# Kernel tuning notes

Hardware: AMD Instinct MI355X
Metric: run time of the kernel (lower is better)

The kernel has to match this reference:

```python
import jax, jax.numpy as jnp
import numpy as np

N = 131072      # nodes
E = 2097152     # edges (avg degree 16)
G = 64          # graphs in batch
D_IN = 64       # input node feature dim
D_E = 2         # raw edge feature dim
H = 128         # hidden dim
OUT = 128       # output dim
L = 3           # num GCN layers
GDIM = 6        # global feature dim
GP = H // 4     # global proj dim = 32
EPS = 1e-5      # BatchNorm eps


def setup_inputs() -> dict:
    key = jax.random.key(0)
    ks = jax.random.split(key, 24)
    s = lambda d: 1.0 / np.sqrt(d)
    return {
        "x": jax.random.normal(ks[0], (N, D_IN), jnp.float32),
        "edge_attr_raw": jax.random.normal(ks[1], (E, D_E), jnp.float32),
        "global_x": jax.random.normal(ks[2], (G, GDIM), jnp.float32),
        "W_in": jax.random.normal(ks[3], (D_IN, H), jnp.float32) * s(D_IN),
        "b_in": jnp.zeros((H,), jnp.float32),
        "W_edge": jax.random.normal(ks[4], (D_E, H), jnp.float32) * s(D_E),
        "b_edge": jnp.zeros((H,), jnp.float32),
        "W_gcn": jax.random.normal(ks[5], (L, H, H), jnp.float32) * s(H),
        "b_gcn": jnp.zeros((L, H), jnp.float32),
        "bn_gamma": jnp.ones((L, H), jnp.float32),
        "bn_beta": jnp.zeros((L, H), jnp.float32),
        "bn_mean": jax.random.normal(ks[6], (L, H), jnp.float32) * 0.1,
        "bn_var": jnp.ones((L, H), jnp.float32) + 0.1 * jax.random.uniform(ks[7], (L, H), jnp.float32),
        "W_gproj": jax.random.normal(ks[8], (GDIM, GP), jnp.float32) * s(GDIM),
        "b_gproj": jnp.zeros((GP,), jnp.float32),
        "W_gcomb": jax.random.normal(ks[9], (H + GP, OUT), jnp.float32) * s(H + GP),
        "b_gcomb": jnp.zeros((OUT,), jnp.float32),
        "row": jax.random.randint(ks[10], (E,), 0, N, jnp.int32),
        "col": jax.random.randint(ks[11], (E,), 0, N, jnp.int32),
        "batch": jnp.sort(jax.random.randint(ks[12], (N,), 0, G, jnp.int32)),
    }


def reference(x, edge_attr_raw, global_x, W_in, b_in, W_edge, b_edge,
              W_gcn, b_gcn, bn_gamma, bn_beta, bn_mean, bn_var,
              W_gproj, b_gproj, W_gcomb, b_gcomb, row, col, batch):
    n = x.shape[0]
    h = x @ W_in + b_in                                   # [N,H]
    ea = edge_attr_raw @ W_edge + b_edge                  # [E,H]
    ones_e = jnp.ones((row.shape[0],), h.dtype)
    deg = jnp.clip(jax.ops.segment_sum(ones_e, row, num_segments=n), 1.0)[:, None]
    for i in range(L):
        msg = h[col] * ea                                 # gather + edge weight [E,H]
        agg = jax.ops.segment_sum(msg, row, num_segments=n) / deg  # scatter-add + norm
        h = h + agg
        h = h @ W_gcn[i] + b_gcn[i]
        # eval-mode BatchNorm (running stats); dropout is identity in eval
        h = (h - bn_mean[i]) * (bn_gamma[i] / jnp.sqrt(bn_var[i] + EPS)) + bn_beta[i]
        h = jax.nn.relu(h)
    # global mean pool per graph
    gsum = jax.ops.segment_sum(h, batch, num_segments=G)
    gcnt = jnp.clip(jax.ops.segment_sum(jnp.ones((n,), h.dtype), batch, num_segments=G), 1.0)[:, None]
    g = gsum / gcnt                                       # [G,H]
    gp = jax.nn.relu(global_x @ W_gproj + b_gproj)        # [G,H//4]
    return jnp.concatenate([g, gp], axis=1) @ W_gcomb + b_gcomb  # [G,OUT]
```

## Files before the change

kernel.cpp:

```cpp
#include <hip/hip_runtime.h>
#include <stdint.h>

#define N_NODES 131072
#define N_EDGES 2097152
#define NG 64
#define HD 128
#define NL 3
#define EPSB 1e-5f

#define BUCKETS 256
#define BSHIFT 9
#define ROWS_PB 512
#define CHUNK 8192
#define NCHUNK (N_EDGES / CHUNK)
#define PAD_SLACK (7 * ROWS_PB)
#define CSR_CAP (N_EDGES + BUCKETS * (PAD_SLACK + 8))
#define TPAD 68

typedef unsigned short ushort_t;
typedef __bf16 bf16x8 __attribute__((ext_vector_type(8)));
typedef float f32x4 __attribute__((ext_vector_type(4)));

__device__ __forceinline__ float bf2f(uint32_t u16) {
    union { uint32_t i; float f; } c; c.i = u16 << 16; return c.f;
}
__device__ __forceinline__ float lo2f(uint32_t u) {
    union { uint32_t i; float f; } c; c.i = u << 16; return c.f;
}
__device__ __forceinline__ float hi2f(uint32_t u) {
    union { uint32_t i; float f; } c; c.i = u & 0xffff0000u; return c.f;
}
__device__ __forceinline__ ushort_t f2bf(float f) {
    union { float f; uint32_t i; } c; c.f = f;
    uint32_t u = c.i;
    uint32_t r = (u + 0x7fffu + ((u >> 16) & 1u)) >> 16;
    return (ushort_t)r;
}
__device__ __forceinline__ float ldf(const void* p, int i, int isb) {
    return isb ? bf2f(((const ushort_t*)p)[i]) : ((const float*)p)[i];
}

__global__ void detect_k(const uint32_t* __restrict__ ea, int* __restrict__ flag) {
    __shared__ int sm[256];
    int t = threadIdx.x;
    int plaus = 0;
    for (int j = 0; j < 16; j++) {
        uint32_t w = ea[t * 16 + j];
        uint32_t e0 = (w >> 7) & 0xFF;
        uint32_t e1 = (w >> 23) & 0xFF;
        plaus += (e0 >= 100 && e0 <= 140) ? 1 : 0;
        plaus += (e1 >= 100 && e1 <= 140) ? 1 : 0;
    }
    sm[t] = plaus;
    __syncthreads();
    for (int o = 128; o > 0; o >>= 1) {
        if (t < o) sm[t] += sm[t + o];
        __syncthreads();
    }
    if (t == 0) flag[0] = (sm[0] * 10 >= 8192 * 9) ? 1 : 0;
}

__global__ void prep_bn(const void* gamma, const void* beta,
                        const void* mean, const void* var,
                        const void* bgcn, float* sc, float* sh,
                        const int* __restrict__ flag) {
    int isb = flag[0];
    int i = blockIdx.x * 128 + threadIdx.x;
    if (i < NL * HD) {
        float g = ldf(gamma, i, isb), b = ldf(beta, i, isb);
        float m = ldf(mean, i, isb), v = ldf(var, i, isb), bb = ldf(bgcn, i, isb);
        float s = g / sqrtf(v + EPSB);
        sc[i] = s;
        sh[i] = (bb - m) * s + b;
    }
}

__global__ void transpose_k(const void* __restrict__ W, ushort_t* __restrict__ WTg,
                            const int* __restrict__ flag) {
    int isb = flag[0];
    int idx = blockIdx.x * 256 + threadIdx.x;
    if (idx < NL * HD * HD) {
        int l = idx >> 14;
        int rem = idx & 16383;
        int k = rem >> 7, n = rem & 127;
        WTg[l * 16384 + n * 128 + k] = f2bf(ldf(W, idx, isb));
    }
}

__global__ __launch_bounds__(256) void bucketA_k(
    const int* __restrict__ row, const int* __restrict__ col,
    const void* __restrict__ ea_raw,
    uint2* __restrict__ staged, uint32_t* __restrict__ cntmat,
    uint32_t* __restrict__ offmat, const int* __restrict__ flag)
{
    __shared__ int hist[256], offs[256], offs_ex[256], cur[256];
    int isb = flag[0];
    int t = threadIdx.x;
    int base = blockIdx.x * CHUNK;
    hist[t] = 0;
    __syncthreads();
#pragma unroll 4
    for (int j = 0; j < 32; j++) {
        int r = row[base + j * 256 + t];
        atomicAdd(&hist[r >> BSHIFT], 1);
    }
    __syncthreads();
    int v = hist[t];
    offs[t] = v;
    __syncthreads();
    for (int o = 1; o < 256; o <<= 1) {
        int u = (t >= o) ? offs[t - o] : 0;
        __syncthreads();
        offs[t] += u;
        __syncthreads();
    }
    offs_ex[t] = offs[t] - v;
    cur[t] = 0;
    cntmat[blockIdx.x * 256 + t] = (uint32_t)v;
    offmat[blockIdx.x * 256 + t] = (uint32_t)(offs[t] - v);
    __syncthreads();
    uint2* slice = staged + (size_t)blockIdx.x * CHUNK;
    for (int j = 0; j < 32; j++) {
        int e = base + j * 256 + t;
        int r = row[e];
        int b = r >> BSHIFT;
        uint32_t packed;
        if (isb) {
            packed = ((const uint32_t*)ea_raw)[e];
        } else {
            const float* f = (const float*)ea_raw + (size_t)e * 2;
            packed = (uint32_t)f2bf(f[0]) | ((uint32_t)f2bf(f[1]) << 16);
        }
        int pos = offs_ex[b] + atomicAdd(&cur[b], 1);
        slice[pos] = make_uint2((uint32_t)(((r & (ROWS_PB - 1)) << 17) | col[e]), packed);
    }
}

__global__ __launch_bounds__(256) void bucketsum_k(const uint32_t* __restrict__ cntmat,
                                                   uint32_t* __restrict__ btot) {
    __shared__ int sm[256];
    int b = blockIdx.x, t = threadIdx.x;
    sm[t] = (int)cntmat[t * 256 + b];
    __syncthreads();
    for (int o = 128; o > 0; o >>= 1) {
        if (t < o) sm[t] += sm[t + o];
        __syncthreads();
    }
    if (t == 0) btot[b] = (uint32_t)sm[0];
}

__global__ __launch_bounds__(256) void scan2_k(const uint32_t* __restrict__ btot,
                                               uint32_t* __restrict__ bbase) {
    __shared__ int sm[256];
    int t = threadIdx.x;
    int v = ((int)btot[t] + PAD_SLACK + 7) & ~7;
    sm[t] = v;
    __syncthreads();
    for (int o = 1; o < 256; o <<= 1) {
        int u = (t >= o) ? sm[t - o] : 0;
        __syncthreads();
        sm[t] += u;
        __syncthreads();
    }
    bbase[t] = (uint32_t)(sm[t] - v);
}

__global__ __launch_bounds__(512) void buildB_k(
    const uint2* __restrict__ staged, const uint32_t* __restrict__ cntmat,
    const uint32_t* __restrict__ offmat, const uint32_t* __restrict__ bbase,
    uint2* __restrict__ csr, int* __restrict__ csr_off, int* __restrict__ deg)
{
    __shared__ int runoff[257];
    __shared__ int runstart[256];
    __shared__ int hist2[512];
    __shared__ int po[512];
    __shared__ int cur2[512];
    int b = blockIdx.x, t = threadIdx.x;

    int myc = 0;
    if (t < 256) {
        myc = (int)cntmat[t * 256 + b];
        runstart[t] = t * CHUNK + (int)offmat[t * 256 + b];
        runoff[t] = myc;
    }
    __syncthreads();
    for (int o = 1; o < 256; o <<= 1) {
        int u = 0;
        if (t < 256 && t >= o) u = runoff[t - o];
        __syncthreads();
        if (t < 256) runoff[t] += u;
        __syncthreads();
    }
    if (t < 256) {
        int incl = runoff[t];
        runoff[t] = incl - myc;
        if (t == 255) runoff[256] = incl;
    }
    hist2[t] = 0;
    cur2[t] = 0;
    __syncthreads();
    int T = runoff[256];

    for (int i = t; i < T; i += 512) {
        int lo = 0, hi = 255;
        while (lo < hi) { int mid = (lo + hi + 1) >> 1; if (runoff[mid] <= i) lo = mid; else hi = mid - 1; }
        uint32_t x = staged[runstart[lo] + (i - runoff[lo])].x;
        atomicAdd(&hist2[x >> 17], 1);
    }
    __syncthreads();

    int pv = (hist2[t] + 7) & ~7;
    po[t] = pv;
    __syncthreads();
    for (int o = 1; o < 512; o <<= 1) {
        int u = (t >= o) ? po[t - o] : 0;
        __syncthreads();
        po[t] += u;
        __syncthreads();
    }
    po[t] -= pv;
    __syncthreads();

    int gbase = (int)bbase[b];
    csr_off[b * ROWS_PB + t] = gbase + po[t];
    deg[b * ROWS_PB + t] = hist2[t];

    for (int i = t; i < T; i += 512) {
        int lo = 0, hi = 255;
        while (lo < hi) { int mid = (lo + hi + 1) >> 1; if (runoff[mid] <= i) lo = mid; else hi = mid - 1; }
        uint2 en = staged[runstart[lo] + (i - runoff[lo])];
        int r = en.x >> 17;
        int pos = po[r] + atomicAdd(&cur2[r], 1);
        csr[gbase + pos] = make_uint2(en.x & 0x1FFFFu, en.y);
    }
    __syncthreads();
    int d = hist2[t], p = (d + 7) & ~7;
    for (int k = d; k < p; k++) csr[gbase + po[t] + k] = make_uint2(N_NODES, 0u);
}

__global__ __launch_bounds__(64, 4) void layer_fused_k(
    const uint32_t* __restrict__ h32,
    const int* __restrict__ csr_off, const int* __restrict__ degv,
    const uint2* __restrict__ csr,
    const void* __restrict__ Wedge, const void* __restrict__ bedge,
    const ushort_t* __restrict__ WTg,
    const float* __restrict__ sc, const float* __restrict__ sh,
    ushort_t* __restrict__ Hout,
    const int* __restrict__ flag)
{
    __shared__ uint32_t tile[16 * TPAD];
    int isb = flag[0];
    int lane = threadIdx.x;
    int quad = lane >> 4, l16 = lane & 15;
    int nodebase = blockIdx.x * 16;

    float w0x = ldf(Wedge, 2 * lane, isb),       w0y = ldf(Wedge, 2 * lane + 1, isb);
    float w1x = ldf(Wedge, 128 + 2 * lane, isb), w1y = ldf(Wedge, 128 + 2 * lane + 1, isb);
    float bex = ldf(bedge, 2 * lane, isb),       bey = ldf(bedge, 2 * lane + 1, isb);

    int dg = degv[nodebase];
    int st = csr_off[nodebase];
    for (int i = 0; i < 16; i++) {
        int dgn = 0, stn = 0;
        if (i < 15) {
            dgn = degv[nodebase + i + 1];
            stn = csr_off[nodebase + i + 1];
        }
        uint32_t hn = h32[(uint32_t)(nodebase + i) * 64 + lane];

        int nit = (dg + 7) >> 3;
        const uint4* gp = (const uint4*)csr + (st >> 1);
        float ax = 0.f, ay = 0.f;
        int it = 0;
        for (; it + 2 <= nit; it += 2) {
            uint4 q0 = gp[0], q1 = gp[1], q2 = gp[2], q3 = gp[3];
            uint4 q4 = gp[4], q5 = gp[5], q6 = gp[6], q7 = gp[7];
            gp += 8;
            uint32_t cols[16] = {q0.x, q0.z, q1.x, q1.z, q2.x, q2.z, q3.x, q3.z,
                                 q4.x, q4.z, q5.x, q5.z, q6.x, q6.z, q7.x, q7.z};
            uint32_t eav[16]  = {q0.y, q0.w, q1.y, q1.w, q2.y, q2.w, q3.y, q3.w,
                                 q4.y, q4.w, q5.y, q5.w, q6.y, q6.w, q7.y, q7.w};
            uint32_t hv[16];
#pragma unroll
            for (int j = 0; j < 16; j++) hv[j] = h32[cols[j] * 64 + lane];
#pragma unroll
            for (int j = 0; j < 16; j++) {
                float a0 = bf2f(eav[j] & 0xffffu);
                float a1 = bf2f(eav[j] >> 16);
                float ex = fmaf(a1, w1x, fmaf(a0, w0x, bex));
                float ey = fmaf(a1, w1y, fmaf(a0, w0y, bey));
                ax = fmaf(lo2f(hv[j]), ex, ax);
                ay = fmaf(hi2f(hv[j]), ey, ay);
            }
        }
        if (it < nit) {
            uint4 q0 = gp[0], q1 = gp[1], q2 = gp[2], q3 = gp[3];
            uint32_t cols[8] = {q0.x, q0.z, q1.x, q1.z, q2.x, q2.z, q3.x, q3.z};
            uint32_t eav[8]  = {q0.y, q0.w, q1.y, q1.w, q2.y, q2.w, q3.y, q3.w};
            uint32_t hv[8];
#pragma unroll
            for (int j = 0; j < 8; j++) hv[j] = h32[cols[j] * 64 + lane];
#pragma unroll
            for (int j = 0; j < 8; j++) {
                float a0 = bf2f(eav[j] & 0xffffu);
                float a1 = bf2f(eav[j] >> 16);
                float ex = fmaf(a1, w1x, fmaf(a0, w0x, bex));
                float ey = fmaf(a1, w1y, fmaf(a0, w0y, bey));
                ax = fmaf(lo2f(hv[j]), ex, ax);
                ay = fmaf(hi2f(hv[j]), ey, ay);
            }
        }
        float inv = 1.0f / (float)(dg > 0 ? dg : 1);
        float tx = lo2f(hn) + ax * inv;
        float ty = hi2f(hn) + ay * inv;
        tile[i * TPAD + lane] = (uint32_t)f2bf(tx) | ((uint32_t)f2bf(ty) << 16);
        dg = dgn; st = stn;
    }

    f32x4 acc[8];
#pragma unroll
    for (int c = 0; c < 8; c++) acc[c] = (f32x4){0.f, 0.f, 0.f, 0.f};

#pragma unroll
    for (int kk = 0; kk < 4; kk++) {
        bf16x8 a = *(const bf16x8*)(tile + l16 * TPAD + kk * 16 + quad * 4);
#pragma unroll
        for (int c = 0; c < 8; c++) {
            bf16x8 b = *(const bf16x8*)(WTg + (c * 16 + l16) * 128 + kk * 32 + quad * 8);
            acc[c] = __builtin_amdgcn_mfma_f32_16x16x32_bf16(a, b, acc[c], 0, 0, 0);
        }
    }
#pragma unroll
    for (int c = 0; c < 8; c++) {
        int gcol = c * 16 + l16;
        float s = sc[gcol], o = sh[gcol];
#pragma unroll
        for (int r = 0; r < 4; r++) {
            float v = fmaxf(fmaf(acc[c][r], s, o), 0.f);
            Hout[(size_t)(nodebase + quad * 4 + r) * 128 + gcol] = f2bf(v);
        }
    }
}

__global__ __launch_bounds__(256) void gemm_in_k(
    const void* __restrict__ X, const void* __restrict__ W,
    const void* __restrict__ bin, ushort_t* __restrict__ Hout,
    const int* __restrict__ flag)
{
    __shared__ ushort_t WT[128 * 72];
    int isb = flag[0];
    int tid = threadIdx.x;
    for (int idx = tid; idx < 64 * 128; idx += 256) {
        int k = idx >> 7, n = idx & 127;
        WT[n * 72 + k] = f2bf(ldf(W, idx, isb));
    }
    __syncthreads();
    int wave = tid >> 6, lane = tid & 63;
    int quad = lane >> 4, l16 = lane & 15;
    int row = blockIdx.x * 64 + wave * 16 + l16;

    f32x4 acc[8];
#pragma unroll
    for (int c = 0; c < 8; c++) acc[c] = (f32x4){0.f, 0.f, 0.f, 0.f};

#pragma unroll
    for (int kk = 0; kk < 2; kk++) {
        int aoff = row * 64 + kk * 32 + quad * 8;
        union { bf16x8 v; ushort_t s[8]; } a;
        if (isb) {
            a.v = *(const bf16x8*)((const ushort_t*)X + aoff);
        } else {
            const float* xf = (const float*)X + aoff;
            f32x4 p0 = *(const f32x4*)xf;
            f32x4 p1 = *(const f32x4*)(xf + 4);
#pragma unroll
            for (int j = 0; j < 4; j++) { a.s[j] = f2bf(p0[j]); a.s[4 + j] = f2bf(p1[j]); }
        }
#pragma unroll
        for (int c = 0; c < 8; c++) {
            bf16x8 b = *(const bf16x8*)(&WT[(c * 16 + l16) * 72 + kk * 32 + quad * 8]);
            acc[c] = __builtin_amdgcn_mfma_f32_16x16x32_bf16(a.v, b, acc[c], 0, 0, 0);
        }
    }
    int rbase = blockIdx.x * 64 + wave * 16 + quad * 4;
#pragma unroll
    for (int c = 0; c < 8; c++) {
        int gcol = c * 16 + l16;
        float bb = ldf(bin, gcol, isb);
#pragma unroll
        for (int r = 0; r < 4; r++) {
            Hout[(rbase + r) * 128 + gcol] = f2bf(acc[c][r] + bb);
        }
    }
}

__global__ __launch_bounds__(128) void pool_k(
    const ushort_t* __restrict__ Hf, const int* __restrict__ batch,
    float* __restrict__ gsum, int* __restrict__ gcnt)
{
    int t = threadIdx.x;
    int n0 = blockIdx.x * 256;
    int n1 = n0 + 256;
    int cur = batch[n0];
    float s = 0.f; int c = 0;
    for (int n = n0; n < n1; n++) {
        int g = batch[n];
        if (g != cur) {
            atomicAdd(&gsum[cur * 128 + t], s);
            if (t == 0) atomicAdd(&gcnt[cur], c);
            s = 0.f; c = 0; cur = g;
        }
        s += bf2f(Hf[n * 128 + t]);
        c++;
    }
    atomicAdd(&gsum[cur * 128 + t], s);
    if (t == 0) atomicAdd(&gcnt[cur], c);
}

__global__ __launch_bounds__(128) void final_k(
    const float* __restrict__ gsum, const int* __restrict__ gcnt,
    const void* __restrict__ gx, const void* __restrict__ Wgp,
    const void* __restrict__ bgp, const void* __restrict__ Wgc,
    const void* __restrict__ bgc, void* __restrict__ out,
    const int* __restrict__ flag)
{
    __shared__ float gm[160];
    int isb = flag[0];
    int g = blockIdx.x, t = threadIdx.x;
    int c = gcnt[g]; if (c < 1) c = 1;
    gm[t] = gsum[g * 128 + t] / (float)c;
    if (t < 32) {
        float a = ldf(bgp, t, isb);
        for (int d = 0; d < 6; d++) a += ldf(gx, g * 6 + d, isb) * ldf(Wgp, d * 32 + t, isb);
        gm[128 + t] = fmaxf(a, 0.f);
    }
    __syncthreads();
    float a = ldf(bgc, t, isb);
    for (int k = 0; k < 160; k++) a += gm[k] * ldf(Wgc, k * 128 + t, isb);
    if (isb) ((ushort_t*)out)[g * 128 + t] = f2bf(a);
    else     ((float*)out)[g * 128 + t] = a;
}

extern "C" void kernel_launch(void* const* d_in, const int* in_sizes, int n_in,
                              void* d_out, int out_size, void* d_ws, size_t ws_size,
                              hipStream_t stream) {
    const void* x       = d_in[0];
    const void* ea_raw  = d_in[1];
    const void* gx      = d_in[2];
    const void* W_in    = d_in[3];
    const void* b_in    = d_in[4];
    const void* W_edge  = d_in[5];
    const void* b_edge  = d_in[6];
    const void* W_gcn   = d_in[7];
    const void* b_gcn   = d_in[8];
    const void* bn_g    = d_in[9];
    const void* bn_b    = d_in[10];
    const void* bn_m    = d_in[11];
    const void* bn_v    = d_in[12];
    const void* W_gproj = d_in[13];
    const void* b_gproj = d_in[14];
    const void* W_gcomb = d_in[15];
    const void* b_gcomb = d_in[16];
    const int* row   = (const int*)d_in[17];
    const int* col   = (const int*)d_in[18];
    const int* batch = (const int*)d_in[19];

    char* ws = (char*)d_ws;
    size_t off = 0;
    float*    gsum    = (float*)(ws + off);    off += (size_t)NG * HD * 4;
    int*      gcnt    = (int*)(ws + off);      off += 256;
    size_t zero_bytes = off;
    int*      flag    = (int*)(ws + off);      off += 256;
    uint32_t* cntmat  = (uint32_t*)(ws + off); off += 256 * 256 * 4;
    uint32_t* offmat  = (uint32_t*)(ws + off); off += 256 * 256 * 4;
    uint32_t* btot    = (uint32_t*)(ws + off); off += 1024;
    uint32_t* bbase   = (uint32_t*)(ws + off); off += 1024;
    int*      csr_off = (int*)(ws + off);      off += (size_t)N_NODES * 4;
    int*      deg     = (int*)(ws + off);      off += (size_t)N_NODES * 4;
    ushort_t* wtg     = (ushort_t*)(ws + off); off += (size_t)NL * HD * HD * 2;
    float*    sc      = (float*)(ws + off);    off += (size_t)NL * HD * 4;
    float*    sh      = (float*)(ws + off);    off += (size_t)NL * HD * 4;
    uint2*    csr     = (uint2*)(ws + off);    off += (size_t)CSR_CAP * 8;
    ushort_t* hA      = (ushort_t*)(ws + off); off += (size_t)(N_NODES + 1) * HD * 2;
    ushort_t* hB      = (ushort_t*)(ws + off); off += (size_t)(N_NODES + 1) * HD * 2;
    uint2*    staged  = (uint2*)hB;

    hipMemsetAsync(ws, 0, zero_bytes, stream);
    hipMemsetAsync(hA + (size_t)N_NODES * HD, 0, HD * 2, stream);
    hipMemsetAsync(hB + (size_t)N_NODES * HD, 0, HD * 2, stream);
    detect_k<<<1, 256, 0, stream>>>((const uint32_t*)ea_raw, flag);
    prep_bn<<<3, 128, 0, stream>>>(bn_g, bn_b, bn_m, bn_v, b_gcn, sc, sh, flag);
    transpose_k<<<(NL * HD * HD + 255) / 256, 256, 0, stream>>>(W_gcn, wtg, flag);

    bucketA_k<<<NCHUNK, 256, 0, stream>>>(row, col, ea_raw, staged, cntmat, offmat, flag);
    bucketsum_k<<<BUCKETS, 256, 0, stream>>>(cntmat, btot);
    scan2_k<<<1, 256, 0, stream>>>(btot, bbase);
    buildB_k<<<BUCKETS, 512, 0, stream>>>(staged, cntmat, offmat, bbase, csr, csr_off, deg);

    gemm_in_k<<<N_NODES / 64, 256, 0, stream>>>(x, W_in, b_in, hA, flag);

    ushort_t* hin = hA;
    ushort_t* hout = hB;
    for (int l = 0; l < NL; l++) {
        layer_fused_k<<<N_NODES / 16, 64, 0, stream>>>(
            (const uint32_t*)hin, csr_off, deg, csr,
            W_edge, b_edge, wtg + (size_t)l * HD * HD, sc + l * HD, sh + l * HD,
            hout, flag);
        ushort_t* tmp = hin; hin = hout; hout = tmp;
    }

    pool_k<<<N_NODES / 256, 128, 0, stream>>>(hin, batch, gsum, gcnt);
    final_k<<<NG, 128, 0, stream>>>(gsum, gcnt, gx, W_gproj, b_gproj,
                                    W_gcomb, b_gcomb, d_out, flag);
}
```

Measured before the change: 667.4 us.

## Replace two-pass bucket sort CSR build with global-atomic counting sort

Builds the CSR with a simple counting sort instead of the bucketed two-pass sort. Per-node degrees come from global atomics, a three-stage scan produces padded offsets, and a fill kernel scatters edges with global atomics into a buffer pre-filled with sentinel entries. This drops the staging buffer, the per-bucket binary searches and the shared-memory histograms. In exchange it uses global atomic contention on random rows and scattered writes, and the order of edges within a row is no longer deterministic.

```diff
diff --git a/kernel.cpp b/kernel.cpp
--- a/kernel.cpp
+++ b/kernel.cpp
@@ -8,13 +8,7 @@
 #define NL 3
 #define EPSB 1e-5f
 
-#define BUCKETS 256
-#define BSHIFT 9
-#define ROWS_PB 512
-#define CHUNK 8192
-#define NCHUNK (N_EDGES / CHUNK)
-#define PAD_SLACK (7 * ROWS_PB)
-#define CSR_CAP (N_EDGES + BUCKETS * (PAD_SLACK + 8))
+#define CSR_CAP (N_EDGES + 7 * N_NODES + 8)
 #define TPAD 68
 
 typedef unsigned short ushort_t;
@@ -87,73 +81,43 @@
     }
 }
 
-__global__ __launch_bounds__(256) void bucketA_k(
-    const int* __restrict__ row, const int* __restrict__ col,
-    const void* __restrict__ ea_raw,
-    uint2* __restrict__ staged, uint32_t* __restrict__ cntmat,
-    uint32_t* __restrict__ offmat, const int* __restrict__ flag)
-{
-    __shared__ int hist[256], offs[256], offs_ex[256], cur[256];
-    int isb = flag[0];
-    int t = threadIdx.x;
-    int base = blockIdx.x * CHUNK;
-    hist[t] = 0;
-    __syncthreads();
-#pragma unroll 4
-    for (int j = 0; j < 32; j++) {
-        int r = row[base + j * 256 + t];
-        atomicAdd(&hist[r >> BSHIFT], 1);
-    }
-    __syncthreads();
-    int v = hist[t];
-    offs[t] = v;
+__global__ __launch_bounds__(256) void degcount_k(const int* __restrict__ row,
+                                                  int* __restrict__ deg) {
+    int t = blockIdx.x * 256 + threadIdx.x;
+#pragma unroll
+    for (int j = 0; j < 4; j++) {
+        atomicAdd(&deg[row[t + j * 524288]], 1);
+    }
+}
+
+__global__ __launch_bounds__(256) void scanA_k(const int* __restrict__ deg,
+                                               int* __restrict__ csr_off,
+                                               uint32_t* __restrict__ btot) {
+    __shared__ int sm[256];
+    int b = blockIdx.x, t = threadIdx.x;
+    int r = b * 512 + 2 * t;
+    int p0 = (deg[r] + 7) & ~7;
+    int p1 = (deg[r + 1] + 7) & ~7;
+    int s = p0 + p1;
+    sm[t] = s;
     __syncthreads();
     for (int o = 1; o < 256; o <<= 1) {
-        int u = (t >= o) ? offs[t - o] : 0;
+        int u = (t >= o) ? sm[t - o] : 0;
         __syncthreads();
-        offs[t] += u;
+        sm[t] += u;
         __syncthreads();
     }
-    offs_ex[t] = offs[t] - v;
-    cur[t] = 0;
-    cntmat[blockIdx.x * 256 + t] = (uint32_t)v;
-    offmat[blockIdx.x * 256 + t] = (uint32_t)(offs[t] - v);
-    __syncthreads();
-    uint2* slice = staged + (size_t)blockIdx.x * CHUNK;
-    for (int j = 0; j < 32; j++) {
-        int e = base + j * 256 + t;
-        int r = row[e];
-        int b = r >> BSHIFT;
-        uint32_t packed;
-        if (isb) {
-            packed = ((const uint32_t*)ea_raw)[e];
-        } else {
-            const float* f = (const float*)ea_raw + (size_t)e * 2;
-            packed = (uint32_t)f2bf(f[0]) | ((uint32_t)f2bf(f[1]) << 16);
-        }
-        int pos = offs_ex[b] + atomicAdd(&cur[b], 1);
-        slice[pos] = make_uint2((uint32_t)(((r & (ROWS_PB - 1)) << 17) | col[e]), packed);
-    }
-}
-
-__global__ __launch_bounds__(256) void bucketsum_k(const uint32_t* __restrict__ cntmat,
-                                                   uint32_t* __restrict__ btot) {
-    __shared__ int sm[256];
-    int b = blockIdx.x, t = threadIdx.x;
-    sm[t] = (int)cntmat[t * 256 + b];
-    __syncthreads();
-    for (int o = 128; o > 0; o >>= 1) {
-        if (t < o) sm[t] += sm[t + o];
-        __syncthreads();
-    }
-    if (t == 0) btot[b] = (uint32_t)sm[0];
-}
-
-__global__ __launch_bounds__(256) void scan2_k(const uint32_t* __restrict__ btot,
+    int base = sm[t] - s;
+    csr_off[r] = base;
+    csr_off[r + 1] = base + p0;
+    if (t == 255) btot[b] = (uint32_t)sm[255];
+}
+
+__global__ __launch_bounds__(256) void scanB_k(const uint32_t* __restrict__ btot,
                                                uint32_t* __restrict__ bbase) {
     __shared__ int sm[256];
     int t = threadIdx.x;
-    int v = ((int)btot[t] + PAD_SLACK + 7) & ~7;
+    int v = (int)btot[t];
     sm[t] = v;
     __syncthreads();
     for (int o = 1; o < 256; o <<= 1) {
@@ -165,77 +129,41 @@
     bbase[t] = (uint32_t)(sm[t] - v);
 }
 
-__global__ __launch_bounds__(512) void buildB_k(
-    const uint2* __restrict__ staged, const uint32_t* __restrict__ cntmat,
-    const uint32_t* __restrict__ offmat, const uint32_t* __restrict__ bbase,
-    uint2* __restrict__ csr, int* __restrict__ csr_off, int* __restrict__ deg)
-{
-    __shared__ int runoff[257];
-    __shared__ int runstart[256];
-    __shared__ int hist2[512];
-    __shared__ int po[512];
-    __shared__ int cur2[512];
+__global__ __launch_bounds__(256) void scanC_k(int* __restrict__ csr_off,
+                                               const uint32_t* __restrict__ bbase) {
     int b = blockIdx.x, t = threadIdx.x;
-
-    int myc = 0;
-    if (t < 256) {
-        myc = (int)cntmat[t * 256 + b];
-        runstart[t] = t * CHUNK + (int)offmat[t * 256 + b];
-        runoff[t] = myc;
-    }
-    __syncthreads();
-    for (int o = 1; o < 256; o <<= 1) {
-        int u = 0;
-        if (t < 256 && t >= o) u = runoff[t - o];
-        __syncthreads();
-        if (t < 256) runoff[t] += u;
-        __syncthreads();
-    }
-    if (t < 256) {
-        int incl = runoff[t];
-        runoff[t] = incl - myc;
-        if (t == 255) runoff[256] = incl;
-    }
-    hist2[t] = 0;
-    cur2[t] = 0;
-    __syncthreads();
-    int T = runoff[256];
-
-    for (int i = t; i < T; i += 512) {
-        int lo = 0, hi = 255;
-        while (lo < hi) { int mid = (lo + hi + 1) >> 1; if (runoff[mid] <= i) lo = mid; else hi = mid - 1; }
-        uint32_t x = staged[runstart[lo] + (i - runoff[lo])].x;
-        atomicAdd(&hist2[x >> 17], 1);
-    }
-    __syncthreads();
-
-    int pv = (hist2[t] + 7) & ~7;
-    po[t] = pv;
-    __syncthreads();
-    for (int o = 1; o < 512; o <<= 1) {
-        int u = (t >= o) ? po[t - o] : 0;
-        __syncthreads();
-        po[t] += u;
-        __syncthreads();
-    }
-    po[t] -= pv;
-    __syncthreads();
-
-    int gbase = (int)bbase[b];
-    csr_off[b * ROWS_PB + t] = gbase + po[t];
-    deg[b * ROWS_PB + t] = hist2[t];
-
-    for (int i = t; i < T; i += 512) {
-        int lo = 0, hi = 255;
-        while (lo < hi) { int mid = (lo + hi + 1) >> 1; if (runoff[mid] <= i) lo = mid; else hi = mid - 1; }
-        uint2 en = staged[runstart[lo] + (i - runoff[lo])];
-        int r = en.x >> 17;
-        int pos = po[r] + atomicAdd(&cur2[r], 1);
-        csr[gbase + pos] = make_uint2(en.x & 0x1FFFFu, en.y);
-    }
-    __syncthreads();
-    int d = hist2[t], p = (d + 7) & ~7;
-    for (int k = d; k < p; k++) csr[gbase + po[t] + k] = make_uint2(N_NODES, 0u);
+    int add = (int)bbase[b];
+    csr_off[b * 512 + 2 * t] += add;
+    csr_off[b * 512 + 2 * t + 1] += add;
+}
+
+__global__ __launch_bounds__(256) void fillsent_k(uint2* __restrict__ csr) {
+    int t = blockIdx.x * 256 + threadIdx.x;
+    uint4 sv = make_uint4(N_NODES, 0u, N_NODES, 0u);
+    uint4* p = (uint4*)csr;
+    for (int i = t; i < CSR_CAP / 2; i += 2048 * 256) p[i] = sv;
+}
+
+__global__ __launch_bounds__(256) void fill_k(
+    const int* __restrict__ row, const int* __restrict__ col,
+    const void* __restrict__ ea_raw, const int* __restrict__ csr_off,
+    int* __restrict__ cur, uint2* __restrict__ csr, const int* __restrict__ flag) {
+    int isb = flag[0];
+    int t = blockIdx.x * 256 + threadIdx.x;
+#pragma unroll
+    for (int j = 0; j < 4; j++) {
+        int e = t + j * 524288;
+        int r = row[e];
+        uint32_t packed;
+        if (isb) {
+            packed = ((const uint32_t*)ea_raw)[e];
+        } else {
+            const float* f = (const float*)ea_raw + (size_t)e * 2;
+            packed = (uint32_t)f2bf(f[0]) | ((uint32_t)f2bf(f[1]) << 16);
+        }
+        int pos = csr_off[r] + atomicAdd(&cur[r], 1);
+        csr[pos] = make_uint2((uint32_t)col[e], packed);
+    }
 }
 
 __global__ __launch_bounds__(64, 4) void layer_fused_k(
@@ -469,33 +397,34 @@
     size_t off = 0;
     float*    gsum    = (float*)(ws + off);    off += (size_t)NG * HD * 4;
     int*      gcnt    = (int*)(ws + off);      off += 256;
+    int*      deg     = (int*)(ws + off);      off += (size_t)N_NODES * 4;
+    int*      cur     = (int*)(ws + off);      off += (size_t)N_NODES * 4;
     size_t zero_bytes = off;
     int*      flag    = (int*)(ws + off);      off += 256;
-    uint32_t* cntmat  = (uint32_t*)(ws + off); off += 256 * 256 * 4;
-    uint32_t* offmat  = (uint32_t*)(ws + off); off += 256 * 256 * 4;
     uint32_t* btot    = (uint32_t*)(ws + off); off += 1024;
     uint32_t* bbase   = (uint32_t*)(ws + off); off += 1024;
     int*      csr_off = (int*)(ws + off);      off += (size_t)N_NODES * 4;
-    int*      deg     = (int*)(ws + off);      off += (size_t)N_NODES * 4;
     ushort_t* wtg     = (ushort_t*)(ws + off); off += (size_t)NL * HD * HD * 2;
     float*    sc      = (float*)(ws + off);    off += (size_t)NL * HD * 4;
     float*    sh      = (float*)(ws + off);    off += (size_t)NL * HD * 4;
     uint2*    csr     = (uint2*)(ws + off);    off += (size_t)CSR_CAP * 8;
     ushort_t* hA      = (ushort_t*)(ws + off); off += (size_t)(N_NODES + 1) * HD * 2;
     ushort_t* hB      = (ushort_t*)(ws + off); off += (size_t)(N_NODES + 1) * HD * 2;
-    uint2*    staged  = (uint2*)hB;
 
     hipMemsetAsync(ws, 0, zero_bytes, stream);
     hipMemsetAsync(hA + (size_t)N_NODES * HD, 0, HD * 2, stream);
     hipMemsetAsync(hB + (size_t)N_NODES * HD, 0, HD * 2, stream);
+
     detect_k<<<1, 256, 0, stream>>>((const uint32_t*)ea_raw, flag);
     prep_bn<<<3, 128, 0, stream>>>(bn_g, bn_b, bn_m, bn_v, b_gcn, sc, sh, flag);
     transpose_k<<<(NL * HD * HD + 255) / 256, 256, 0, stream>>>(W_gcn, wtg, flag);
 
-    bucketA_k<<<NCHUNK, 256, 0, stream>>>(row, col, ea_raw, staged, cntmat, offmat, flag);
-    bucketsum_k<<<BUCKETS, 256, 0, stream>>>(cntmat, btot);
-    scan2_k<<<1, 256, 0, stream>>>(btot, bbase);
-    buildB_k<<<BUCKETS, 512, 0, stream>>>(staged, cntmat, offmat, bbase, csr, csr_off, deg);
+    fillsent_k<<<2048, 256, 0, stream>>>(csr);
+    degcount_k<<<2048, 256, 0, stream>>>(row, deg);
+    scanA_k<<<256, 256, 0, stream>>>(deg, csr_off, btot);
+    scanB_k<<<1, 256, 0, stream>>>(btot, bbase);
+    scanC_k<<<256, 256, 0, stream>>>(csr_off, bbase);
+    fill_k<<<2048, 256, 0, stream>>>(row, col, ea_raw, csr_off, cur, csr, flag);
 
     gemm_in_k<<<N_NODES / 64, 256, 0, stream>>>(x, W_in, b_in, hA, flag);
 
```

Measured after the change: 830.4 us. +24.4%, slower.
